# Optimization experiments

Hardware: AMD Instinct MI355X
Metric: run time of the kernel (lower is better)

Reference implementation:

```python
import jax, jax.numpy as jnp
import numpy as np

N = 50000      # total nodes (10 graphs x 5000 nodes)
E = 800000     # edges
C_IN = 128
C_H = 64
NL = 9         # num_layers - 1 GCN layers


def setup_inputs() -> dict:
    key = jax.random.key(0)
    ks = jax.random.split(key, 10)
    x = jax.random.normal(ks[0], (N, C_IN), jnp.float32)
    edge_index = jax.random.randint(ks[1], (2, E), 0, N, dtype=jnp.int32)
    # GCN layer weights (stored as [in, out] so h @ W matches torch's x @ W.T)
    W0 = jax.random.normal(ks[2], (C_IN, C_H), jnp.float32) / np.sqrt(C_IN)
    b0 = jnp.zeros((C_H,), jnp.float32)
    Ws = jax.random.normal(ks[3], (NL - 1, C_H, C_H), jnp.float32) / np.sqrt(C_H)
    bs = jnp.zeros((NL - 1, C_H), jnp.float32)
    Wn = jax.random.normal(ks[4], (C_H, C_H), jnp.float32) / np.sqrt(C_H)   # node_transform
    Wp = jax.random.normal(ks[5], (C_H, C_H), jnp.float32) / np.sqrt(C_H)   # neig_transform
    Wa = jax.random.normal(ks[6], (2 * C_H, 1), jnp.float32) / np.sqrt(2 * C_H)  # aggr_transform
    return {"x": x, "edge_index": edge_index, "W0": W0, "b0": b0, "Ws": Ws,
            "bs": bs, "Wn": Wn, "Wp": Wp, "Wa": Wa, "n": 5000}


def reference(x, edge_index, W0, b0, Ws, bs, Wn, Wp, Wa, n):
    num_nodes = x.shape[0]
    src, dst = edge_index[0], edge_index[1]
    # GCN symmetric normalization with self loops (PyG gcn_norm defaults)
    deg = jax.ops.segment_sum(jnp.ones(src.shape[0], x.dtype), dst,
                              num_segments=num_nodes) + 1.0
    dinv = jax.lax.rsqrt(deg)
    enorm = dinv[src] * dinv[dst]        # per-edge norm
    snorm = dinv * dinv                  # self-loop norm

    h = x
    for i in range(NL):
        W = W0 if i == 0 else Ws[i - 1]
        b_ = b0 if i == 0 else bs[i - 1]
        hw = h @ W                                                   # [N, C_H]
        agg = jax.ops.segment_sum(hw[src] * enorm[:, None], dst,
                                  num_segments=num_nodes)
        h = jax.nn.relu(agg + hw * snorm[:, None] + b_)

    h = h @ Wn                                                       # node_transform
    b = num_nodes // n
    batch = jnp.repeat(jnp.arange(b), n)                             # graph id per node
    pool = jax.ops.segment_sum(h, batch, num_segments=b)             # global_add_pool
    rep = (pool @ Wp)[batch]                                         # repeated_pool
    cat = jnp.concatenate([h, rep], axis=1)                          # [N, 2*C_H]
    return jnp.tanh(jax.nn.relu(cat) @ Wa)                           # [N, 1]
```

## Files before the change

### kernel.cpp

```cpp
#include <hip/hip_runtime.h>
#include <hip/hip_bf16.h>

#define N_NODES 50000
#define N_EDGES 800000
#define C_IN    128
#define C_H     64
#define C_HU    32
#define N_LAYER 9
#define N_GRAPH 10
#define N_PER_G 5000
#define NSB     ((N_NODES + 255) / 256)
#define NPB     16
#define NPX     (N_NODES / 8)

typedef unsigned int  u32;
typedef unsigned short u16;
typedef __bf16 bf16x8 __attribute__((ext_vector_type(8)));
typedef float  f32x4  __attribute__((ext_vector_type(4)));

__device__ __forceinline__ float bflo(u32 u) { return __uint_as_float(u << 16); }
__device__ __forceinline__ float bfhi(u32 u) { return __uint_as_float(u & 0xffff0000u); }
__device__ __forceinline__ u16 f2bf(float f) {
    u32 u = __float_as_uint(f);
    u32 r = u + 0x7fffu + ((u >> 16) & 1u);
    return (u16)(r >> 16);
}
__device__ __forceinline__ void add8(float* acc, uint4 v) {
    acc[0] += bflo(v.x); acc[1] += bfhi(v.x);
    acc[2] += bflo(v.y); acc[3] += bfhi(v.y);
    acc[4] += bflo(v.z); acc[5] += bfhi(v.z);
    acc[6] += bflo(v.w); acc[7] += bfhi(v.w);
}


__global__ __launch_bounds__(256) void count_kernel(const int* __restrict__ dst,
                                                    int* __restrict__ cnt) {
    int grp = blockIdx.x & 7;
    int blk = blockIdx.x >> 3;
    int lo = grp * NPX, hi = lo + NPX;
    for (int i = blk * 256 + threadIdx.x; i < N_EDGES; i += 128 * 256) {
        int d = dst[i];
        if (d >= lo && d < hi) atomicAdd(&cnt[d], 1);
    }
}

__global__ __launch_bounds__(256) void bsum_kernel(const int* __restrict__ cnt,
                                                   int* __restrict__ bsum) {
    int i = blockIdx.x * 256 + threadIdx.x;
    int v = (i < N_NODES) ? cnt[i] : 0;
#pragma unroll
    for (int off = 32; off; off >>= 1) v += __shfl_down(v, off);
    __shared__ int s[4];
    if ((threadIdx.x & 63) == 0) s[threadIdx.x >> 6] = v;
    __syncthreads();
    if (threadIdx.x == 0) bsum[blockIdx.x] = s[0] + s[1] + s[2] + s[3];
}

__global__ __launch_bounds__(256) void scan2_kernel(const int* __restrict__ cnt,
                                                    const int* __restrict__ bsum,
                                                    int* __restrict__ rowStart,
                                                    int* __restrict__ cursor,
                                                    float* __restrict__ dinv) {
    int b = blockIdx.x, t = threadIdx.x;
    int v = (t < b) ? bsum[t] : 0;
#pragma unroll
    for (int off = 32; off; off >>= 1) v += __shfl_down(v, off);
    __shared__ int sw[4];
    __shared__ int soff;
    if ((t & 63) == 0) sw[t >> 6] = v;
    __syncthreads();
    if (t == 0) soff = sw[0] + sw[1] + sw[2] + sw[3];

    int i = b * 256 + t;
    int c = (i < N_NODES) ? cnt[i] : 0;
    __shared__ int sd[256];
    sd[t] = c;
    __syncthreads();
#pragma unroll
    for (int off = 1; off < 256; off <<= 1) {
        int x = sd[t];
        int y = (t >= off) ? sd[t - off] : 0;
        __syncthreads();
        sd[t] = x + y;
        __syncthreads();
    }
    if (i < N_NODES) {
        int rs = soff + sd[t] - c;
        rowStart[i] = rs;
        cursor[i] = rs;
        dinv[i] = rsqrtf((float)c + 1.0f);
    }
}

__global__ __launch_bounds__(256) void scatter_kernel(const int* __restrict__ src,
                                                      const int* __restrict__ dst,
                                                      int* __restrict__ cursor,
                                                      u16* __restrict__ csr16) {
    int grp = blockIdx.x & 7;
    int blk = blockIdx.x >> 3;
    int lo = grp * NPX, hi = lo + NPX;
    for (int i = blk * 256 + threadIdx.x; i < N_EDGES; i += 128 * 256) {
        int d = dst[i];
        if (d >= lo && d < hi) {
            int p = atomicAdd(&cursor[d], 1);
            csr16[p] = (u16)src[i];
        }
    }
}


__global__ __launch_bounds__(256) void gemm0_kernel(const float* __restrict__ x,
                                                    const float* __restrict__ W0,
                                                    const float* __restrict__ dinv,
                                                    u16* __restrict__ out) {
    __shared__ float Wlds[C_IN * C_H];
    for (int t = threadIdx.x; t < (C_IN * C_H) / 4; t += 256)
        *(float4*)&Wlds[t * 4] = *(const float4*)&W0[t * 4];
    __syncthreads();

    int wid = threadIdx.x >> 6, lane = threadIdx.x & 63;
    int lr = lane & 15, lg = lane >> 4;

    bf16x8 bfr[4][4];
#pragma unroll
    for (int ct = 0; ct < 4; ct++)
#pragma unroll
        for (int kk = 0; kk < 4; kk++)
#pragma unroll
            for (int j = 0; j < 8; j++)
                bfr[ct][kk][j] = (__bf16)Wlds[(kk * 32 + lg * 8 + j) * C_H + ct * 16 + lr];

    for (int t = blockIdx.x * 4 + wid; t < N_NODES / 16; t += gridDim.x * 4) {
        int row0 = t * 16;
        bf16x8 af[4];
#pragma unroll
        for (int kk = 0; kk < 4; kk++) {
            const float* xp = x + (size_t)(row0 + lr) * C_IN + kk * 32 + lg * 8;
            float4 p0 = *(const float4*)xp;
            float4 p1 = *(const float4*)(xp + 4);
            af[kk][0] = (__bf16)p0.x; af[kk][1] = (__bf16)p0.y;
            af[kk][2] = (__bf16)p0.z; af[kk][3] = (__bf16)p0.w;
            af[kk][4] = (__bf16)p1.x; af[kk][5] = (__bf16)p1.y;
            af[kk][6] = (__bf16)p1.z; af[kk][7] = (__bf16)p1.w;
        }
        f32x4 acc[4];
#pragma unroll
        for (int ct = 0; ct < 4; ct++) acc[ct] = (f32x4){0.f, 0.f, 0.f, 0.f};
#pragma unroll
        for (int ct = 0; ct < 4; ct++)
#pragma unroll
            for (int kk = 0; kk < 4; kk++)
                acc[ct] = __builtin_amdgcn_mfma_f32_16x16x32_bf16(af[kk], bfr[ct][kk], acc[ct], 0, 0, 0);
#pragma unroll
        for (int reg = 0; reg < 4; reg++) {
            int rr = row0 + lg * 4 + reg;
            float dv = dinv[rr];
#pragma unroll
            for (int ct = 0; ct < 4; ct++)
                out[(size_t)rr * C_H + ct * 16 + lr] = f2bf(acc[ct][reg] * dv);
        }
    }
}


#define CLOAD(dst, n, d, b_)                                                      \
    {                                                                             \
        int e_ = (b_) + 8 * (d) + g;                                              \
        int s_ = csr16[sq##n + ((e_ < dq##n) ? e_ : 0)];                          \
        dst = (e_ < dq##n) ? s_ : N_NODES;                                        \
    }

#define ROWAS(v_, s_) v_ = *(const uint4*)(hw + (size_t)(s_) * C_HU + r * 4);

#define RED(Aq)                                                                   \
    _Pragma("unroll")                                                             \
    for (int c = 0; c < 8; c++) {                                                 \
        Aq[c] += __shfl_xor(Aq[c], 8);                                            \
        Aq[c] += __shfl_xor(Aq[c], 16);                                           \
        Aq[c] += __shfl_xor(Aq[c], 32);                                           \
    }

#define EPILOG(q, iq, Aq)                                                         \
    {                                                                             \
        float di = dinv[iq];                                                      \
        uint4 sv = *(const uint4*)(hw + (size_t)(iq) * C_HU + r * 4);             \
        if (g == 0) {                                                             \
            float h0 = fmaxf(di * (Aq[0] + bflo(sv.x)) + b8[0], 0.f);             \
            float h1 = fmaxf(di * (Aq[1] + bfhi(sv.x)) + b8[1], 0.f);             \
            float h2 = fmaxf(di * (Aq[2] + bflo(sv.y)) + b8[2], 0.f);             \
            float h3 = fmaxf(di * (Aq[3] + bfhi(sv.y)) + b8[3], 0.f);             \
            float h4 = fmaxf(di * (Aq[4] + bflo(sv.z)) + b8[4], 0.f);             \
            float h5 = fmaxf(di * (Aq[5] + bfhi(sv.z)) + b8[5], 0.f);             \
            float h6 = fmaxf(di * (Aq[6] + bflo(sv.w)) + b8[6], 0.f);             \
            float h7 = fmaxf(di * (Aq[7] + bfhi(sv.w)) + b8[7], 0.f);             \
            uint4 pk;                                                             \
            pk.x = (u32)f2bf(h0) | ((u32)f2bf(h1) << 16);                         \
            pk.y = (u32)f2bf(h2) | ((u32)f2bf(h3) << 16);                         \
            pk.z = (u32)f2bf(h4) | ((u32)f2bf(h5) << 16);                         \
            pk.w = (u32)f2bf(h6) | ((u32)f2bf(h7) << 16);                         \
            int n_ = wave * 4 + q;                                                \
            int rs_ = r ^ (n_ & 7);                \
            *(uint4*)&hbuf32[n_ * 32 + rs_ * 4] = pk;                             \
        }                                                                         \
    }

__global__ __launch_bounds__(256) void layer_kernel(const u32* __restrict__ hw,
                                                    const int* __restrict__ rowStart,
                                                    const int* __restrict__ cnt,
                                                    const u16* __restrict__ csr16,
                                                    const float* __restrict__ dinv,
                                                    const float* __restrict__ bias,
                                                    const float* __restrict__ Wnext,
                                                    int scaled,
                                                    u16* __restrict__ out) {
    __shared__ u32 hbuf32[NPB * C_HU];

    int wave = threadIdx.x >> 6, lane = threadIdx.x & 63;
    int g = lane >> 3;
    int r = lane & 7;
    int jblock = blockIdx.x * NPB;
    int jbase = jblock + wave * 4;

    int i0 = jbase + 0, i1 = jbase + 1, i2 = jbase + 2, i3 = jbase + 3;
    int sq0 = rowStart[i0], sq1 = rowStart[i1], sq2 = rowStart[i2], sq3 = rowStart[i3];
    int dq0 = cnt[i0], dq1 = cnt[i1], dq2 = cnt[i2], dq3 = cnt[i3];
    int dmax = max(max(dq0, dq1), max(dq2, dq3));

    float A0[8] = {0.f,0.f,0.f,0.f,0.f,0.f,0.f,0.f};
    float A1[8] = {0.f,0.f,0.f,0.f,0.f,0.f,0.f,0.f};
    float A2[8] = {0.f,0.f,0.f,0.f,0.f,0.f,0.f,0.f};
    float A3[8] = {0.f,0.f,0.f,0.f,0.f,0.f,0.f,0.f};

    int s00, s01, s10, s11, s20, s21, s30, s31;
    CLOAD(s00, 0, 0, 0) CLOAD(s01, 0, 1, 0)
    CLOAD(s10, 1, 0, 0) CLOAD(s11, 1, 1, 0)
    CLOAD(s20, 2, 0, 0) CLOAD(s21, 2, 1, 0)
    CLOAD(s30, 3, 0, 0) CLOAD(s31, 3, 1, 0)

    uint4 v00, v01, v10, v11, v20, v21, v30, v31;
    ROWAS(v00, s00) ROWAS(v01, s01)
    ROWAS(v10, s10) ROWAS(v11, s11)
    ROWAS(v20, s20) ROWAS(v21, s21)
    ROWAS(v30, s30) ROWAS(v31, s31)

    int t00, t01, t10, t11, t20, t21, t30, t31;
    CLOAD(t00, 0, 0, 16) CLOAD(t01, 0, 1, 16)
    CLOAD(t10, 1, 0, 16) CLOAD(t11, 1, 1, 16)
    CLOAD(t20, 2, 0, 16) CLOAD(t21, 2, 1, 16)
    CLOAD(t30, 3, 0, 16) CLOAD(t31, 3, 1, 16)

    for (int base = 0; base < dmax; base += 16) {
        uint4 n00, n01, n10, n11, n20, n21, n30, n31;
        ROWAS(n00, t00) ROWAS(n01, t01)
        ROWAS(n10, t10) ROWAS(n11, t11)
        ROWAS(n20, t20) ROWAS(n21, t21)
        ROWAS(n30, t30) ROWAS(n31, t31)
        int nb = base + 32;
        int u00, u01, u10, u11, u20, u21, u30, u31;
        CLOAD(u00, 0, 0, nb) CLOAD(u01, 0, 1, nb)
        CLOAD(u10, 1, 0, nb) CLOAD(u11, 1, 1, nb)
        CLOAD(u20, 2, 0, nb) CLOAD(u21, 2, 1, nb)
        CLOAD(u30, 3, 0, nb) CLOAD(u31, 3, 1, nb)
        add8(A0, v00); add8(A0, v01);
        add8(A1, v10); add8(A1, v11);
        add8(A2, v20); add8(A2, v21);
        add8(A3, v30); add8(A3, v31);
        v00 = n00; v01 = n01; v10 = n10; v11 = n11;
        v20 = n20; v21 = n21; v30 = n30; v31 = n31;
        t00 = u00; t01 = u01; t10 = u10; t11 = u11;
        t20 = u20; t21 = u21; t30 = u30; t31 = u31;
    }

    RED(A0) RED(A1) RED(A2) RED(A3)

    float b8[8];
    *(float4*)&b8[0] = *(const float4*)(bias + r * 8);
    *(float4*)&b8[4] = *(const float4*)(bias + r * 8 + 4);

    EPILOG(0, i0, A0)
    EPILOG(1, i1, A1)
    EPILOG(2, i2, A2)
    EPILOG(3, i3, A3)

    __syncthreads();

    {
        int ct = wave;
        int lr = lane & 15, lg = lane >> 4;
        bf16x8 bw[2];
#pragma unroll
        for (int ks = 0; ks < 2; ks++)
#pragma unroll
            for (int j = 0; j < 8; j++)
                bw[ks][j] = (__bf16)Wnext[(ks * 32 + lg * 8 + j) * C_H + ct * 16 + lr];
        const u16* hb = (const u16*)hbuf32;
        bf16x8 ah[2];
#pragma unroll
        for (int ks = 0; ks < 2; ks++) {
            int c = lg + 4 * ks;
            int cs = c ^ (lr & 7);
            ah[ks] = *(const bf16x8*)&hb[lr * C_H + cs * 8];
        }
        f32x4 accv = (f32x4){0.f, 0.f, 0.f, 0.f};
        accv = __builtin_amdgcn_mfma_f32_16x16x32_bf16(ah[0], bw[0], accv, 0, 0, 0);
        accv = __builtin_amdgcn_mfma_f32_16x16x32_bf16(ah[1], bw[1], accv, 0, 0, 0);
        float4 dv4 = *(const float4*)(dinv + jblock + lg * 4);
        float dvs[4] = {dv4.x, dv4.y, dv4.z, dv4.w};
#pragma unroll
        for (int reg = 0; reg < 4; reg++) {
            int nn = jblock + lg * 4 + reg;
            float sc_ = scaled ? dvs[reg] : 1.0f;
            out[(size_t)nn * C_H + ct * 16 + lr] = f2bf(accv[reg] * sc_);
        }
    }
}


__global__ __launch_bounds__(256) void pool_kernel(const u16* __restrict__ hn,
                                                   float* __restrict__ poolbuf) {
    int g = blockIdx.x >> 4;
    int s = blockIdx.x & 15;
    int lane = threadIdx.x & 63;
    int rg = threadIdx.x >> 6;
    int stream = s * 4 + rg;
    float acc = 0.f;
    for (int r = stream; r < N_PER_G; r += 64)
        acc += bflo((u32)hn[(size_t)(g * N_PER_G + r) * C_H + lane]);
    __shared__ float red[4][C_H];
    red[rg][lane] = acc;
    __syncthreads();
    if (rg == 0) {
        float t = red[0][lane] + red[1][lane] + red[2][lane] + red[3][lane];
        atomicAdd(&poolbuf[g * C_H + lane], t);
    }
}

__global__ void poolwp_kernel(const float* __restrict__ poolbuf,
                              const float* __restrict__ Wp,
                              float* __restrict__ poolwp) {
    int g = blockIdx.x, c = threadIdx.x;
    float o = 0.f;
#pragma unroll 8
    for (int k = 0; k < C_H; k++) o += poolbuf[g * C_H + k] * Wp[k * C_H + c];
    poolwp[g * C_H + c] = o;
}

__global__ __launch_bounds__(256) void final_kernel(const u16* __restrict__ hn,
                                                    const float* __restrict__ poolwp,
                                                    const float* __restrict__ Wa,
                                                    float* __restrict__ out, int n) {
    int wave = threadIdx.x >> 6, lane = threadIdx.x & 63;
    int i = blockIdx.x * 4 + wave;
    if (i >= n) return;
    int g = i / N_PER_G;
    float v = fmaxf(bflo((u32)hn[(size_t)i * C_H + lane]), 0.f) * Wa[lane]
            + fmaxf(poolwp[g * C_H + lane], 0.f) * Wa[C_H + lane];
#pragma unroll
    for (int off = 32; off; off >>= 1) v += __shfl_down(v, off);
    if (lane == 0) out[i] = tanhf(v);
}


extern "C" void kernel_launch(void* const* d_in, const int* in_sizes, int n_in,
                              void* d_out, int out_size, void* d_ws, size_t ws_size,
                              hipStream_t stream) {
    const float* x   = (const float*)d_in[0];
    const int*   ei  = (const int*)d_in[1];
    const float* W0  = (const float*)d_in[2];
    const float* b0  = (const float*)d_in[3];
    const float* Ws  = (const float*)d_in[4];
    const float* bs  = (const float*)d_in[5];
    const float* Wn  = (const float*)d_in[6];
    const float* Wp  = (const float*)d_in[7];
    const float* Wa  = (const float*)d_in[8];
    float* out = (float*)d_out;

    const int* e_src = ei;
    const int* e_dst = ei + N_EDGES;

    size_t off = 0;
    auto alloc = [&](size_t bytes) { size_t o = off; off = (off + bytes + 255) & ~(size_t)255; return o; };
    char* ws = (char*)d_ws;
    int*   cnt      = (int*)  (ws + alloc(N_NODES * 4));
    int*   rowStart = (int*)  (ws + alloc(N_NODES * 4));
    int*   cursor   = (int*)  (ws + alloc(N_NODES * 4));
    float* dinv     = (float*)(ws + alloc(N_NODES * 4));
    int*   bsum     = (int*)  (ws + alloc(NSB * 4));
    u16*   csr16    = (u16*)  (ws + alloc((size_t)(N_EDGES + 64) * 2));
    u16*   bufA     = (u16*)  (ws + alloc((size_t)(N_NODES + 1) * C_H * 2));
    u16*   bufB     = (u16*)  (ws + alloc((size_t)(N_NODES + 1) * C_H * 2));
    float* poolbuf  = (float*)(ws + alloc(N_GRAPH * C_H * 4));
    float* poolwp   = (float*)(ws + alloc(N_GRAPH * C_H * 4));

    hipMemsetAsync(cnt, 0, N_NODES * 4, stream);
    hipMemsetAsync(poolbuf, 0, N_GRAPH * C_H * 4, stream);
    hipMemsetAsync(bufA + (size_t)N_NODES * C_H, 0, C_H * 2, stream);
    hipMemsetAsync(bufB + (size_t)N_NODES * C_H, 0, C_H * 2, stream);

    count_kernel<<<1024, 256, 0, stream>>>(e_dst, cnt);
    bsum_kernel<<<NSB, 256, 0, stream>>>(cnt, bsum);
    scan2_kernel<<<NSB, 256, 0, stream>>>(cnt, bsum, rowStart, cursor, dinv);
    scatter_kernel<<<1024, 256, 0, stream>>>(e_src, e_dst, cursor, csr16);

    gemm0_kernel<<<391, 256, 0, stream>>>(x, W0, dinv, bufA);

    const int LB = N_NODES / NPB;
    for (int k = 0; k < N_LAYER; k++) {
        const u16* hin  = (k & 1) ? bufB : bufA;
        u16*       hout = (k & 1) ? bufA : bufB;
        const float* bias  = (k == 0) ? b0 : (bs + (k - 1) * C_H);
        const float* Wnext = (k < N_LAYER - 1) ? (Ws + k * C_H * C_H) : Wn;
        int scaled = (k < N_LAYER - 1) ? 1 : 0;
        layer_kernel<<<LB, 256, 0, stream>>>((const u32*)hin, rowStart, cnt, csr16,
                                             dinv, bias, Wnext, scaled, hout);
    }
    const u16* hn = bufB;

    pool_kernel<<<N_GRAPH * 16, 256, 0, stream>>>(hn, poolbuf);
    poolwp_kernel<<<N_GRAPH, C_H, 0, stream>>>(poolbuf, Wp, poolwp);
    final_kernel<<<N_NODES / 4, 256, 0, stream>>>(hn, poolwp, Wa, out, N_NODES);
}
```

Baseline: 433.9 us.

## Pre-pack layer weights into MFMA bf16 layout and vectorize edge preprocessing

```diff
diff --git a/kernel.cpp b/kernel.cpp
--- a/kernel.cpp
+++ b/kernel.cpp
@@ -33,14 +33,17 @@
 }
 
 
-__global__ __launch_bounds__(256) void count_kernel(const int* __restrict__ dst,
+__global__ __launch_bounds__(256) void count_kernel(const int4* __restrict__ dst4,
                                                     int* __restrict__ cnt) {
     int grp = blockIdx.x & 7;
     int blk = blockIdx.x >> 3;
     int lo = grp * NPX, hi = lo + NPX;
-    for (int i = blk * 256 + threadIdx.x; i < N_EDGES; i += 128 * 256) {
-        int d = dst[i];
-        if (d >= lo && d < hi) atomicAdd(&cnt[d], 1);
+    for (int q = blk * 256 + threadIdx.x; q < N_EDGES / 4; q += 128 * 256) {
+        int4 d = dst4[q];
+        if (d.x >= lo && d.x < hi) atomicAdd(&cnt[d.x], 1);
+        if (d.y >= lo && d.y < hi) atomicAdd(&cnt[d.y], 1);
+        if (d.z >= lo && d.z < hi) atomicAdd(&cnt[d.z], 1);
+        if (d.w >= lo && d.w < hi) atomicAdd(&cnt[d.w], 1);
     }
 }
 
@@ -92,20 +95,34 @@
     }
 }
 
-__global__ __launch_bounds__(256) void scatter_kernel(const int* __restrict__ src,
-                                                      const int* __restrict__ dst,
+__global__ __launch_bounds__(256) void scatter_kernel(const int4* __restrict__ src4,
+                                                      const int4* __restrict__ dst4,
                                                       int* __restrict__ cursor,
                                                       u16* __restrict__ csr16) {
     int grp = blockIdx.x & 7;
     int blk = blockIdx.x >> 3;
     int lo = grp * NPX, hi = lo + NPX;
-    for (int i = blk * 256 + threadIdx.x; i < N_EDGES; i += 128 * 256) {
-        int d = dst[i];
-        if (d >= lo && d < hi) {
-            int p = atomicAdd(&cursor[d], 1);
-            csr16[p] = (u16)src[i];
-        }
-    }
+    for (int q = blk * 256 + threadIdx.x; q < N_EDGES / 4; q += 128 * 256) {
+        int4 d = dst4[q];
+        int4 s = src4[q];
+        if (d.x >= lo && d.x < hi) { int p = atomicAdd(&cursor[d.x], 1); csr16[p] = (u16)s.x; }
+        if (d.y >= lo && d.y < hi) { int p = atomicAdd(&cursor[d.y], 1); csr16[p] = (u16)s.y; }
+        if (d.z >= lo && d.z < hi) { int p = atomicAdd(&cursor[d.z], 1); csr16[p] = (u16)s.z; }
+        if (d.w >= lo && d.w < hi) { int p = atomicAdd(&cursor[d.w], 1); csr16[p] = (u16)s.w; }
+    }
+}
+
+
+__global__ __launch_bounds__(256) void wtrans_kernel(const float* __restrict__ Ws,
+                                                     const float* __restrict__ Wn,
+                                                     u16* __restrict__ Wt) {
+    int i = blockIdx.x * 256 + threadIdx.x;
+    if (i >= 9 * 4096) return;
+    int layer = i >> 12, t = i & 4095;
+    int k = t >> 6, c = t & 63;
+    const float* W = (layer < 8) ? (Ws + layer * 4096) : Wn;
+    int ct = c >> 4, lr = c & 15, ks = k >> 5, lg = (k >> 3) & 3, j = k & 7;
+    Wt[layer * 4096 + (((ct * 2 + ks) * 4 + lg) * 16 + lr) * 8 + j] = f2bf(W[k * 64 + c]);
 }
 
 
@@ -180,19 +197,18 @@
         Aq[c] += __shfl_xor(Aq[c], 32);                                           \
     }
 
-#define EPILOG(q, iq, Aq)                                                         \
+#define EPILOG(q, iq, Aq, svq)                                                    \
     {                                                                             \
         float di = dinv[iq];                                                      \
-        uint4 sv = *(const uint4*)(hw + (size_t)(iq) * C_HU + r * 4);             \
         if (g == 0) {                                                             \
-            float h0 = fmaxf(di * (Aq[0] + bflo(sv.x)) + b8[0], 0.f);             \
-            float h1 = fmaxf(di * (Aq[1] + bfhi(sv.x)) + b8[1], 0.f);             \
-            float h2 = fmaxf(di * (Aq[2] + bflo(sv.y)) + b8[2], 0.f);             \
-            float h3 = fmaxf(di * (Aq[3] + bfhi(sv.y)) + b8[3], 0.f);             \
-            float h4 = fmaxf(di * (Aq[4] + bflo(sv.z)) + b8[4], 0.f);             \
-            float h5 = fmaxf(di * (Aq[5] + bfhi(sv.z)) + b8[5], 0.f);             \
-            float h6 = fmaxf(di * (Aq[6] + bflo(sv.w)) + b8[6], 0.f);             \
-            float h7 = fmaxf(di * (Aq[7] + bfhi(sv.w)) + b8[7], 0.f);             \
+            float h0 = fmaxf(di * (Aq[0] + bflo(svq.x)) + b8[0], 0.f);            \
+            float h1 = fmaxf(di * (Aq[1] + bfhi(svq.x)) + b8[1], 0.f);            \
+            float h2 = fmaxf(di * (Aq[2] + bflo(svq.y)) + b8[2], 0.f);            \
+            float h3 = fmaxf(di * (Aq[3] + bfhi(svq.y)) + b8[3], 0.f);            \
+            float h4 = fmaxf(di * (Aq[4] + bflo(svq.z)) + b8[4], 0.f);            \
+            float h5 = fmaxf(di * (Aq[5] + bfhi(svq.z)) + b8[5], 0.f);            \
+            float h6 = fmaxf(di * (Aq[6] + bflo(svq.w)) + b8[6], 0.f);            \
+            float h7 = fmaxf(di * (Aq[7] + bfhi(svq.w)) + b8[7], 0.f);            \
             uint4 pk;                                                             \
             pk.x = (u32)f2bf(h0) | ((u32)f2bf(h1) << 16);                         \
             pk.y = (u32)f2bf(h2) | ((u32)f2bf(h3) << 16);                         \
@@ -210,7 +226,7 @@
                                                     const u16* __restrict__ csr16,
                                                     const float* __restrict__ dinv,
                                                     const float* __restrict__ bias,
-                                                    const float* __restrict__ Wnext,
+                                                    const u16* __restrict__ wtL,
                                                     int scaled,
                                                     u16* __restrict__ out) {
     __shared__ u32 hbuf32[NPB * C_HU];
@@ -225,6 +241,9 @@
     int sq0 = rowStart[i0], sq1 = rowStart[i1], sq2 = rowStart[i2], sq3 = rowStart[i3];
     int dq0 = cnt[i0], dq1 = cnt[i1], dq2 = cnt[i2], dq3 = cnt[i3];
     int dmax = max(max(dq0, dq1), max(dq2, dq3));
+
+    uint4 sv0, sv1, sv2, sv3;
+    ROWAS(sv0, i0) ROWAS(sv1, i1) ROWAS(sv2, i2) ROWAS(sv3, i3)
 
     float A0[8] = {0.f,0.f,0.f,0.f,0.f,0.f,0.f,0.f};
     float A1[8] = {0.f,0.f,0.f,0.f,0.f,0.f,0.f,0.f};
@@ -277,22 +296,18 @@
     *(float4*)&b8[0] = *(const float4*)(bias + r * 8);
     *(float4*)&b8[4] = *(const float4*)(bias + r * 8 + 4);
 
-    EPILOG(0, i0, A0)
-    EPILOG(1, i1, A1)
-    EPILOG(2, i2, A2)
-    EPILOG(3, i3, A3)
+    EPILOG(0, i0, A0, sv0)
+    EPILOG(1, i1, A1, sv1)
+    EPILOG(2, i2, A2, sv2)
+    EPILOG(3, i3, A3, sv3)
 
     __syncthreads();
 
     {
         int ct = wave;
         int lr = lane & 15, lg = lane >> 4;
-        bf16x8 bw[2];
-#pragma unroll
-        for (int ks = 0; ks < 2; ks++)
-#pragma unroll
-            for (int j = 0; j < 8; j++)
-                bw[ks][j] = (__bf16)Wnext[(ks * 32 + lg * 8 + j) * C_H + ct * 16 + lr];
+        bf16x8 bw0 = *(const bf16x8*)&wtL[(((ct * 2 + 0) * 4 + lg) * 16 + lr) * 8];
+        bf16x8 bw1 = *(const bf16x8*)&wtL[(((ct * 2 + 1) * 4 + lg) * 16 + lr) * 8];
         const u16* hb = (const u16*)hbuf32;
         bf16x8 ah[2];
 #pragma unroll
@@ -302,8 +317,8 @@
             ah[ks] = *(const bf16x8*)&hb[lr * C_H + cs * 8];
         }
         f32x4 accv = (f32x4){0.f, 0.f, 0.f, 0.f};
-        accv = __builtin_amdgcn_mfma_f32_16x16x32_bf16(ah[0], bw[0], accv, 0, 0, 0);
-        accv = __builtin_amdgcn_mfma_f32_16x16x32_bf16(ah[1], bw[1], accv, 0, 0, 0);
+        accv = __builtin_amdgcn_mfma_f32_16x16x32_bf16(ah[0], bw0, accv, 0, 0, 0);
+        accv = __builtin_amdgcn_mfma_f32_16x16x32_bf16(ah[1], bw1, accv, 0, 0, 0);
         float4 dv4 = *(const float4*)(dinv + jblock + lg * 4);
         float dvs[4] = {dv4.x, dv4.y, dv4.z, dv4.w};
 #pragma unroll
@@ -387,6 +402,7 @@
     float* dinv     = (float*)(ws + alloc(N_NODES * 4));
     int*   bsum     = (int*)  (ws + alloc(NSB * 4));
     u16*   csr16    = (u16*)  (ws + alloc((size_t)(N_EDGES + 64) * 2));
+    u16*   Wt       = (u16*)  (ws + alloc((size_t)9 * 4096 * 2));
     u16*   bufA     = (u16*)  (ws + alloc((size_t)(N_NODES + 1) * C_H * 2));
     u16*   bufB     = (u16*)  (ws + alloc((size_t)(N_NODES + 1) * C_H * 2));
     float* poolbuf  = (float*)(ws + alloc(N_GRAPH * C_H * 4));
@@ -397,10 +413,12 @@
     hipMemsetAsync(bufA + (size_t)N_NODES * C_H, 0, C_H * 2, stream);
     hipMemsetAsync(bufB + (size_t)N_NODES * C_H, 0, C_H * 2, stream);
 
-    count_kernel<<<1024, 256, 0, stream>>>(e_dst, cnt);
+    count_kernel<<<1024, 256, 0, stream>>>((const int4*)e_dst, cnt);
     bsum_kernel<<<NSB, 256, 0, stream>>>(cnt, bsum);
     scan2_kernel<<<NSB, 256, 0, stream>>>(cnt, bsum, rowStart, cursor, dinv);
-    scatter_kernel<<<1024, 256, 0, stream>>>(e_src, e_dst, cursor, csr16);
+    scatter_kernel<<<1024, 256, 0, stream>>>((const int4*)e_src, (const int4*)e_dst,
+                                             cursor, csr16);
+    wtrans_kernel<<<144, 256, 0, stream>>>(Ws, Wn, Wt);
 
     gemm0_kernel<<<391, 256, 0, stream>>>(x, W0, dinv, bufA);
 
@@ -408,11 +426,11 @@
     for (int k = 0; k < N_LAYER; k++) {
         const u16* hin  = (k & 1) ? bufB : bufA;
         u16*       hout = (k & 1) ? bufA : bufB;
-        const float* bias  = (k == 0) ? b0 : (bs + (k - 1) * C_H);
-        const float* Wnext = (k < N_LAYER - 1) ? (Ws + k * C_H * C_H) : Wn;
+        const float* bias = (k == 0) ? b0 : (bs + (k - 1) * C_H);
+        const u16* wtL = Wt + k * 4096;
         int scaled = (k < N_LAYER - 1) ? 1 : 0;
         layer_kernel<<<LB, 256, 0, stream>>>((const u32*)hin, rowStart, cnt, csr16,
-                                             dinv, bias, Wnext, scaled, hout);
+                                             dinv, bias, wtL, scaled, hout);
     }
     const u16* hn = bufB;
 
```

After: 477.7 us. +10.1%, slower.
